# Kernel optimization log

Hardware: AMD Instinct MI355X
Metric: run time of the kernel (lower is better)

The kernel has to match this reference:

```python
import jax, jax.numpy as jnp
import numpy as np

# Qwen3.5 GatedDeltaNet dims
B, T, HID = 2, 2048, 2048
HK, HV, DK, DV, KW = 16, 32, 128, 128, 4   # k-heads, v-heads, head dims, conv kernel
R = HV // HK                                # GQA repeat factor = 2
KEY_DIM = HK * DK                           # 2048
VAL_DIM = HV * DV                           # 4096
CONV_DIM = 2 * KEY_DIM + VAL_DIM            # 8192
EPS = 1e-6


def setup_inputs() -> dict:
    key = jax.random.key(0)
    ks = jax.random.split(key, 10)
    w = lambda k, shape, s=0.02: (jax.random.normal(k, shape) * s).astype(jnp.float32)
    A = jax.random.uniform(ks[8], (HV,), minval=1e-3, maxval=16.0)
    return {
        "hidden_states": jax.random.normal(ks[0], (B, T, HID), jnp.float32),
        "W_qkv": w(ks[1], (HID, CONV_DIM)),
        "W_z": w(ks[2], (HID, VAL_DIM)),
        "W_b": w(ks[3], (HID, HV)),
        "W_a": w(ks[4], (HID, HV)),
        "conv_w": w(ks[5], (CONV_DIM, KW), 0.5),   # depthwise causal conv taps
        "dt_bias": jnp.ones((HV,), jnp.float32),
        "A_log": jnp.log(A).astype(jnp.float32),
        "norm_weight": jnp.ones((DV,), jnp.float32),
        "W_out": w(ks[9], (VAL_DIM, HID)),
    }


def _forward(hidden_states, W_qkv, W_z, W_b, W_a, conv_w, dt_bias, A_log, norm_weight, W_out):
    x = hidden_states
    # --- projections ---
    qkv = x @ W_qkv                                    # [B,T,CONV_DIM]
    z = x @ W_z                                        # [B,T,VAL_DIM]
    beta = jax.nn.sigmoid(x @ W_b)                     # [B,T,HV]
    alpha = x @ W_a                                    # [B,T,HV]
    g = -jnp.exp(A_log) * jax.nn.softplus(alpha + dt_bias)  # [B,T,HV] (log-decay <= 0)

    # --- fix_query_key_value_ordering: per-k-head interleaved layout ---
    qkv = qkv.reshape(B, T, HK, 2 * DK + R * DV)
    q, k, v = jnp.split(qkv, [DK, 2 * DK], axis=3)
    mixed = jnp.concatenate([q.reshape(B, T, -1), k.reshape(B, T, -1), v.reshape(B, T, -1)], axis=-1)

    # --- causal depthwise short conv (kernel 4) + SiLU ---
    xp = jnp.pad(mixed, ((0, 0), (KW - 1, 0), (0, 0)))
    conv = sum(conv_w[:, i] * xp[:, i:i + T, :] for i in range(KW))
    conv = jax.nn.silu(conv)

    q, k, v = jnp.split(conv, [KEY_DIM, 2 * KEY_DIM], axis=-1)
    q = q.reshape(B, T, HK, DK)
    k = k.reshape(B, T, HK, DK)
    v = v.reshape(B, T, HV, DV)
    gate = z.reshape(B, T, HV, DV)

    # GQA: repeat q,k heads to match v heads
    q = jnp.repeat(q, R, axis=2)                       # [B,T,HV,DK]
    k = jnp.repeat(k, R, axis=2)

    # l2-norm q,k (use_qk_l2norm_in_kernel=True) and default scale 1/sqrt(DK)
    q = q / jnp.sqrt(jnp.sum(q * q, axis=-1, keepdims=True) + 1e-6)
    k = k / jnp.sqrt(jnp.sum(k * k, axis=-1, keepdims=True) + 1e-6)
    q = q * (DK ** -0.5)

    # --- gated delta rule recurrence (scan over time) ---
    # state S: [B,HV,DK,DV];  S_t = a_t*S_{t-1} + k_t (beta_t*(v_t - (a_t*S_{t-1})^T k_t))^T
    def step(S, inp):
        qt, kt, vt, gt, bt = inp                       # [B,HV,DK],[B,HV,DK],[B,HV,DV],[B,HV],[B,HV]
        S = S * jnp.exp(gt)[:, :, None, None]
        kv = jnp.einsum('bhk,bhkv->bhv', kt, S)
        delta = bt[..., None] * (vt - kv)              # [B,HV,DV]
        S = S + kt[..., None] * delta[:, :, None, :]
        o = jnp.einsum('bhk,bhkv->bhv', qt, S)
        return S, o

    tfirst = lambda a: jnp.moveaxis(a, 1, 0)           # [T,B,...]
    S0 = jnp.zeros((B, HV, DK, DV), q.dtype)
    _, o = jax.lax.scan(step, S0, (tfirst(q), tfirst(k), tfirst(v), tfirst(g), tfirst(beta)))
    o = jnp.moveaxis(o, 0, 1)                          # [B,T,HV,DV]

    # --- gated RMSNorm: rmsnorm(o) * silu(gate) * weight ---
    var = jnp.mean(o * o, axis=-1, keepdims=True)
    o = o * jax.lax.rsqrt(var + EPS)
    o = o * jax.nn.silu(gate)
    o = o * norm_weight

    return o.reshape(B, T, VAL_DIM) @ W_out            # [B,T,HID]


def reference(hidden_states, W_qkv, W_z, W_b, W_a, conv_w, dt_bias, A_log, norm_weight, W_out):
    return _forward(hidden_states, W_qkv, W_z, W_b, W_a, conv_w, dt_bias, A_log, norm_weight, W_out)
```

## Files before the change

### kernel.cpp

```cpp
#include <hip/hip_runtime.h>


#define T_LEN 2048
#define MROWS 4096
#define CPAD 65

typedef __bf16 bf16x8 __attribute__((ext_vector_type(8)));
typedef float f32x4 __attribute__((ext_vector_type(4)));

#define MFMA(a, b, c) __builtin_amdgcn_mfma_f32_16x16x32_bf16((a), (b), (c), 0, 0, 0)

__device__ __forceinline__ unsigned short f2bf(float f) {
  unsigned int u = __float_as_uint(f);
  unsigned int r = (u + 0x7fffu + ((u >> 16) & 1u)) >> 16;
  return (unsigned short)r;
}
__device__ __forceinline__ float bf2f(unsigned short u) {
  return __uint_as_float(((unsigned int)u) << 16);
}
__device__ __forceinline__ void gload_lds16(const void* g, void* l) {
  __builtin_amdgcn_global_load_lds(
      (const __attribute__((address_space(1))) unsigned int*)g,
      (__attribute__((address_space(3))) unsigned int*)l, 16, 0, 0);
}

__global__ __launch_bounds__(256) void f32_to_bf16_vec(const float* __restrict__ src,
                                                       unsigned short* __restrict__ dst,
                                                       int n4) {
  int i = blockIdx.x * 256 + threadIdx.x;
  if (i >= n4) return;
  float4 v = ((const float4*)src)[i];
  ushort4 o;
  o.x = f2bf(v.x); o.y = f2bf(v.y); o.z = f2bf(v.z); o.w = f2bf(v.w);
  ((ushort4*)dst)[i] = o;
}

__global__ __launch_bounds__(256) void transpose_f2b(const float* __restrict__ src,
                                                     unsigned short* __restrict__ dst,
                                                     int R, int C) {
  __shared__ float tile[32][33];
  int tx = threadIdx.x & 31, ty = threadIdx.x >> 5;
  int c0 = blockIdx.x * 32, r0 = blockIdx.y * 32;
  #pragma unroll
  for (int i = ty; i < 32; i += 8)
    tile[i][tx] = src[(size_t)(r0 + i) * C + c0 + tx];
  __syncthreads();
  #pragma unroll
  for (int i = ty; i < 32; i += 8)
    dst[(size_t)(c0 + i) * R + r0 + tx] = f2bf(tile[tx][i]);
}

template <int OUTBF, int BN>
__global__ __launch_bounds__(512, 2) void gemm256(const unsigned short* __restrict__ A, int lda,
                                                  const unsigned short* __restrict__ Bt, int ldb,
                                                  void* __restrict__ Cv, int ldc,
                                                  int M, int N, int K) {
  constexpr int BUFSZ = 16384 + BN * 64;
  constexpr int BISS = BN / 64;
  constexpr int IS = 4 + BISS;
  constexpr int WMv = (BN == 256) ? 2 : 4;
  constexpr int MSUB = 256 / (WMv * 16);
  constexpr int MSPAN = 256 / WMv;

  __shared__ unsigned short lds[2 * BUFSZ];

  const int mtiles = M >> 8;
  const int nwg = gridDim.x;
  const int orig = blockIdx.x;
  const int q = nwg >> 3, r = nwg & 7;
  const int xcd = orig & 7, idx = orig >> 3;
  const int swz = (xcd < r ? xcd * (q + 1) : r * (q + 1) + (xcd - r) * q) + idx;
  const int m0 = (swz % mtiles) * 256;
  const int n0 = (swz / mtiles) * BN;

  const int tid = threadIdx.x, lane = tid & 63, wv = tid >> 6;
  const int wm = (BN == 256) ? (wv >> 2) : (wv >> 1);
  const int wn = (BN == 256) ? (wv & 3) : (wv & 1);
  const int l15 = lane & 15, l4 = lane >> 4;

  f32x4 acc[MSUB][4];
  #pragma unroll
  for (int i = 0; i < MSUB; i++)
    #pragma unroll
    for (int j = 0; j < 4; j++) acc[i][j] = f32x4{0.f, 0.f, 0.f, 0.f};

  const int NT = K >> 6;

  auto STAGE = [&](int kt) {
    unsigned short* base = lds + (kt & 1) * BUFSZ;
    const int k0 = kt << 6;
    #pragma unroll
    for (int is = 0; is < 4; is++) {
      int ow = is * 8192 + wv * 1024;
      int o = ow + lane * 16;
      int row = o >> 7, colB = o & 127;
      int scol = colB ^ ((row & 7) << 4);
      gload_lds16(A + (size_t)(m0 + row) * lda + k0 + (scol >> 1), base + (ow >> 1));
    }
    #pragma unroll
    for (int is = 0; is < BISS; is++) {
      int ow = is * 8192 + wv * 1024;
      int o = ow + lane * 16;
      int row = o >> 7, colB = o & 127;
      int scol = colB ^ ((row & 7) << 4);
      gload_lds16(Bt + (size_t)(n0 + row) * ldb + k0 + (scol >> 1), base + 16384 + (ow >> 1));
    }
  };

  STAGE(0);
  if (NT > 1) STAGE(1);
  if constexpr (IS == 8) asm volatile("s_waitcnt vmcnt(8)" ::: "memory");
  else                   asm volatile("s_waitcnt vmcnt(6)" ::: "memory");
  __builtin_amdgcn_sched_barrier(0);
  __builtin_amdgcn_s_barrier();
  __builtin_amdgcn_sched_barrier(0);

  for (int t = 0; t < NT; t++) {
    const unsigned short* Abuf = lds + (t & 1) * BUFSZ;
    const unsigned short* Bbuf = Abuf + 16384;
    bf16x8 bF[4][2];
    #pragma unroll
    for (int n = 0; n < 4; n++) {
      int rb = wn * 64 + n * 16 + l15;
      int sw = (rb & 7) << 4;
      #pragma unroll
      for (int ks = 0; ks < 2; ks++) {
        int colB = (ks * 32 + l4 * 8) * 2;
        bF[n][ks] = *(const bf16x8*)(Bbuf + rb * 64 + ((colB ^ sw) >> 1));
      }
    }
    __builtin_amdgcn_s_setprio(1);
    #pragma unroll
    for (int m = 0; m < MSUB; m++) {
      int ra = wm * MSPAN + m * 16 + l15;
      int sw = (ra & 7) << 4;
      int c0b = l4 * 16;
      bf16x8 a0 = *(const bf16x8*)(Abuf + ra * 64 + ((c0b ^ sw) >> 1));
      bf16x8 a1 = *(const bf16x8*)(Abuf + ra * 64 + (((64 + c0b) ^ sw) >> 1));
      #pragma unroll
      for (int n = 0; n < 4; n++) {
        acc[m][n] = MFMA(a0, bF[n][0], acc[m][n]);
        acc[m][n] = MFMA(a1, bF[n][1], acc[m][n]);
      }
    }
    __builtin_amdgcn_s_setprio(0);
    __builtin_amdgcn_sched_barrier(0);
    __builtin_amdgcn_s_barrier();
    __builtin_amdgcn_sched_barrier(0);
    if (t + 2 < NT) STAGE(t + 2);
    if (t + 1 < NT) {
      if (t + 2 < NT) {
        if constexpr (IS == 8) asm volatile("s_waitcnt vmcnt(8)" ::: "memory");
        else                   asm volatile("s_waitcnt vmcnt(6)" ::: "memory");
      } else {
        asm volatile("s_waitcnt vmcnt(0)" ::: "memory");
      }
      __builtin_amdgcn_sched_barrier(0);
      __builtin_amdgcn_s_barrier();
      __builtin_amdgcn_sched_barrier(0);
    }
  }

  #pragma unroll
  for (int m = 0; m < MSUB; m++) {
    int grow = m0 + wm * MSPAN + m * 16 + l4 * 4;
    #pragma unroll
    for (int n = 0; n < 4; n++) {
      int gcol = n0 + wn * 64 + n * 16 + l15;
      if (OUTBF) {
        unsigned short* cp = (unsigned short*)Cv + (size_t)grow * ldc + gcol;
        #pragma unroll
        for (int rr = 0; rr < 4; rr++) cp[(size_t)rr * ldc] = f2bf(acc[m][n][rr]);
      } else {
        float* cp = (float*)Cv + (size_t)grow * ldc + gcol;
        #pragma unroll
        for (int rr = 0; rr < 4; rr++) cp[(size_t)rr * ldc] = acc[m][n][rr];
      }
    }
  }
}

template <int OUTBF>
__global__ __launch_bounds__(256) void gemm_bf16(const unsigned short* __restrict__ A, int lda,
                                                 const unsigned short* __restrict__ Bt, int ldb,
                                                 void* __restrict__ Cv, int ldc,
                                                 int M, int N, int K) {
  __shared__ unsigned short As[128 * 64];
  __shared__ unsigned short Bs[128 * 64];
  const int tid = threadIdx.x, lane = tid & 63, wv = tid >> 6;
  const int wr = wv >> 1, wc = wv & 1;
  const int m0 = blockIdx.y * 128, n0 = blockIdx.x * 128;
  const int lrow8 = lane >> 3;
  const int lk8 = (lane & 7) * 8;

  f32x4 acc[4][4];
  #pragma unroll
  for (int i = 0; i < 4; i++)
    #pragma unroll
    for (int j = 0; j < 4; j++) acc[i][j] = f32x4{0.f, 0.f, 0.f, 0.f};

  for (int k0 = 0; k0 < K; k0 += 64) {
    #pragma unroll
    for (int j = 0; j < 4; ++j) {
      int chunk = j * 4 + wv;
      int r = chunk * 8 + lrow8;
      gload_lds16(A + (size_t)(m0 + r) * lda + k0 + lk8, (void*)(As + chunk * 512));
      gload_lds16(Bt + (size_t)(n0 + r) * ldb + k0 + lk8, (void*)(Bs + chunk * 512));
    }
    __syncthreads();
    #pragma unroll
    for (int half = 0; half < 2; ++half) {
      int ko = half * 32 + (lane >> 4) * 8;
      bf16x8 af[4], bfr[4];
      #pragma unroll
      for (int i = 0; i < 4; i++) {
        int ra = wr * 64 + i * 16 + (lane & 15);
        af[i] = *(const bf16x8*)(As + ra * 64 + ko);
        int rb = wc * 64 + i * 16 + (lane & 15);
        bfr[i] = *(const bf16x8*)(Bs + rb * 64 + ko);
      }
      #pragma unroll
      for (int i = 0; i < 4; i++)
        #pragma unroll
        for (int j = 0; j < 4; j++)
          acc[i][j] = MFMA(af[i], bfr[j], acc[i][j]);
    }
    __syncthreads();
  }
  int cr4 = (lane >> 4) * 4;
  int cc = lane & 15;
  #pragma unroll
  for (int i = 0; i < 4; i++) {
    int row = m0 + wr * 64 + i * 16 + cr4;
    #pragma unroll
    for (int j = 0; j < 4; j++) {
      int col = n0 + wc * 64 + j * 16 + cc;
      if (OUTBF) {
        unsigned short* cp = (unsigned short*)Cv + (size_t)row * ldc + col;
        #pragma unroll
        for (int r = 0; r < 4; r++) cp[(size_t)r * ldc] = f2bf(acc[i][j][r]);
      } else {
        float* cp = (float*)Cv + (size_t)row * ldc + col;
        #pragma unroll
        for (int r = 0; r < 4; r++) cp[(size_t)r * ldc] = acc[i][j][r];
      }
    }
  }
}

__global__ __launch_bounds__(256) void beta_g_kernel(const unsigned short* __restrict__ ba,
                                                     const float* __restrict__ A_log,
                                                     const float* __restrict__ dt_bias,
                                                     unsigned short* __restrict__ betab,
                                                     float* __restrict__ g) {
  int i = blockIdx.x * 256 + threadIdx.x;
  int row = i >> 5, hv = i & 31;
  float rb = bf2f(ba[(size_t)row * 128 + hv]);
  float ra = bf2f(ba[(size_t)row * 128 + 32 + hv]);
  betab[i] = f2bf(1.f / (1.f + expf(-rb)));
  float xg = ra + dt_bias[hv];
  float sp = (xg > 20.f) ? xg : log1pf(expf(xg));
  g[i] = -expf(A_log[hv]) * sp;
}

__global__ __launch_bounds__(256) void conv_kernel(const unsigned short* __restrict__ qkv,
                                                   const float* __restrict__ conv_w,
                                                   unsigned short* __restrict__ out) {
  const int seg = blockIdx.x, tt = blockIdx.y, b = blockIdx.z;
  const int tid = threadIdx.x;
  const int c0 = seg * 128;
  const bool isq = seg < 16;
  int scb;
  if (isq) scb = seg * 512;
  else if (seg < 32) scb = (seg - 16) * 512 + 128;
  else scb = ((seg - 32) >> 1) * 512 + 256 + ((seg - 32) & 1) * 128;

  __shared__ unsigned short raw[35][136];
  __shared__ float cw[4][132];

  for (int i = tid; i < 512; i += 256) {
    int cl = i >> 2, tap = i & 3;
    cw[tap][cl] = conv_w[(size_t)(c0 + cl) * 4 + tap];
  }
  const int t0 = tt * 32;
  for (int i = tid; i < 560; i += 256) {
    int row = i >> 4, col = (i & 15) * 8;
    int gt = t0 - 3 + row;
    uint4 v = make_uint4(0u, 0u, 0u, 0u);
    if (gt >= 0) v = *(const uint4*)(qkv + (size_t)(b * T_LEN + gt) * 8192 + scb + col);
    *(uint4*)(&raw[row][col]) = v;
  }
  __syncthreads();
  const int s = tid >> 3, dg = tid & 7;
  union RawU { uint4 v[2]; unsigned short h[16]; };
  RawU u[4];
  #pragma unroll
  for (int i = 0; i < 4; i++) {
    const uint4* p = (const uint4*)&raw[s + i][dg * 16];
    u[i].v[0] = p[0]; u[i].v[1] = p[1];
  }
  float vals[16]; float ss = 0.f;
  #pragma unroll
  for (int j = 0; j < 16; j++) {
    float a = 0.f;
    #pragma unroll
    for (int i = 0; i < 4; i++) a = fmaf(cw[i][dg * 16 + j], bf2f(u[i].h[j]), a);
    a = a / (1.f + expf(-a));
    vals[j] = a; ss += a * a;
  }
  if (seg < 32) {
    ss += __shfl_xor(ss, 1); ss += __shfl_xor(ss, 2); ss += __shfl_xor(ss, 4);
    float sc = rsqrtf(ss + 1e-6f);
    if (isq) sc *= 0.08838834764831845f;
    #pragma unroll
    for (int j = 0; j < 16; j++) vals[j] *= sc;
  }
  union { uint4 v[2]; unsigned short h[16]; } ov;
  #pragma unroll
  for (int j = 0; j < 16; j++) ov.h[j] = f2bf(vals[j]);
  unsigned short* op = out + (size_t)(b * T_LEN + t0 + s) * 8192 + c0 + dg * 16;
  *(uint4*)(op) = ov.v[0];
  *(uint4*)(op + 8) = ov.v[1];
}

__global__ __launch_bounds__(256) void prep_kernel(const unsigned short* __restrict__ conv,
                                                   const float* __restrict__ g,
                                                   const unsigned short* __restrict__ betab,
                                                   unsigned short* __restrict__ M1g,
                                                   unsigned short* __restrict__ M2g,
                                                   unsigned char* __restrict__ vecs) {
  const int c = blockIdx.x, bh = blockIdx.y;
  const int b = bh >> 5, hv = bh & 31, hk = hv >> 1;
  const int bhc = bh * 32 + c;
  const int tid = threadIdx.x, lane = tid & 63, wv = tid >> 6;
  const int r0 = b * T_LEN + c * 64;

  __shared__ unsigned short Kb[128 * 72];
  __shared__ unsigned short Qb[64 * 136];
  __shared__ float Ab[64 * CPAD];
  __shared__ unsigned short Pb[64 * 72];
  __shared__ float Gs[64], Ls[64], SCs[64], BLs[64];

  if (wv == 0) {
    float gt = g[(size_t)(r0 + lane) * 32 + hv];
    #pragma unroll
    for (int d = 1; d < 64; d <<= 1) {
      float o = __shfl_up(gt, (unsigned)d, 64);
      if (lane >= d) gt += o;
    }
    float GC = __shfl(gt, 63, 64);
    float lam = expf(gt);
    float beta = bf2f(betab[(size_t)(r0 + lane) * 32 + hv]);
    Gs[lane] = gt; Ls[lane] = lam;
    SCs[lane] = expf(GC - gt);
    BLs[lane] = beta;
    unsigned short* vb16 = (unsigned short*)(vecs + (size_t)bhc * 272);
    vb16[lane] = f2bf(beta * lam);
    vb16[64 + lane] = f2bf(lam);
    if (lane == 0) *(float*)(vecs + (size_t)bhc * 272 + 256) = expf(GC);
  }
  const unsigned short* Kg = conv + (size_t)r0 * 8192 + 2048 + hk * 128;
  const unsigned short* Qg = conv + (size_t)r0 * 8192 + hk * 128;
  for (int u = tid; u < 1024; u += 256) {
    int row = u >> 4, col = (u & 15) * 8;
    *(uint4*)(&Kb[row * 136 + col]) = *(const uint4*)(Kg + (size_t)row * 8192 + col);
    *(uint4*)(&Qb[row * 136 + col]) = *(const uint4*)(Qg + (size_t)row * 8192 + col);
  }
  __syncthreads();

  {
    f32x4 akk[4], aqk[4];
    #pragma unroll
    for (int st = 0; st < 4; st++) { akk[st] = f32x4{0,0,0,0}; aqk[st] = f32x4{0,0,0,0}; }
    int trow = wv * 16 + (lane & 15);
    int klo = (lane >> 4) * 8;
    #pragma unroll
    for (int ks = 0; ks < 4; ks++) {
      int ko = ks * 32 + klo;
      bf16x8 ak = *(const bf16x8*)(&Kb[trow * 136 + ko]);
      bf16x8 aq = *(const bf16x8*)(&Qb[trow * 136 + ko]);
      #pragma unroll
      for (int st = 0; st < 4; st++) {
        bf16x8 bk = *(const bf16x8*)(&Kb[(st * 16 + (lane & 15)) * 136 + ko]);
        akk[st] = MFMA(ak, bk, akk[st]);
        aqk[st] = MFMA(aq, bk, aqk[st]);
      }
    }
    int orow = wv * 16 + (lane >> 4) * 4;
    int oc = lane & 15;
    #pragma unroll
    for (int st = 0; st < 4; st++)
      #pragma unroll
      for (int r = 0; r < 4; r++) {
        int t = orow + r, ssv = st * 16 + oc;
        float e = expf(fminf(Gs[t] - Gs[ssv], 0.f));
        Ab[t * CPAD + ssv] = (ssv < t) ? BLs[t] * e * akk[st][r] : (ssv == t ? 1.f : 0.f);
        Pb[t * 72 + ssv] = f2bf((ssv <= t) ? e * aqk[st][r] : 0.f);
      }
  }
  __syncthreads();

  {
    unsigned short ktv[32];
    int dk = tid >> 1, tb = (tid & 1) * 32;
    #pragma unroll
    for (int i = 0; i < 32; i++)
      ktv[i] = f2bf(bf2f(Kb[(tb + i) * 136 + dk]) * SCs[tb + i]);
    __syncthreads();
    #pragma unroll
    for (int i = 0; i < 32; i++) Kb[dk * 72 + tb + i] = ktv[i];
  }
  __syncthreads();

  float* XT = (float*)Qb;
  if (wv == 0) {
    XT[lane * CPAD + 0] = (lane == 0) ? 1.f : 0.f;
    for (int t = 1; t < 64; t++) {
      float a0 = 0.f, a1 = 0.f, a2 = 0.f, a3 = 0.f;
      int sI = 0;
      for (; sI + 4 <= t; sI += 4) {
        a0 = fmaf(Ab[t * CPAD + sI],     XT[lane * CPAD + sI],     a0);
        a1 = fmaf(Ab[t * CPAD + sI + 1], XT[lane * CPAD + sI + 1], a1);
        a2 = fmaf(Ab[t * CPAD + sI + 2], XT[lane * CPAD + sI + 2], a2);
        a3 = fmaf(Ab[t * CPAD + sI + 3], XT[lane * CPAD + sI + 3], a3);
      }
      for (; sI < t; sI++) a0 = fmaf(Ab[t * CPAD + sI], XT[lane * CPAD + sI], a0);
      XT[lane * CPAD + t] = ((lane == t) ? 1.f : 0.f) - (a0 + a1 + (a2 + a3));
    }
  }
  __syncthreads();

  unsigned short* XTb = (unsigned short*)Ab;
  for (int e = tid; e < 4096; e += 256) {
    int j = e >> 6, sI = e & 63;
    XTb[j * 72 + sI] = f2bf(XT[j * CPAD + sI]);
  }
  __syncthreads();

  for (int tt = wv * 12; tt < wv * 12 + 12; tt++) {
    f32x4 acc = f32x4{0, 0, 0, 0};
    const unsigned short* Abase;
    int mrow, jc;
    if (tt < 16) { mrow = (tt >> 2) * 16; jc = (tt & 3) * 16; Abase = Pb + mrow * 72; }
    else { int i2 = tt - 16; mrow = (i2 >> 2) * 16; jc = (i2 & 3) * 16; Abase = Kb + mrow * 72; }
    #pragma unroll
    for (int ks = 0; ks < 2; ks++) {
      int so = ks * 32 + (lane >> 4) * 8;
      bf16x8 af = *(const bf16x8*)(Abase + (lane & 15) * 72 + so);
      bf16x8 bfv = *(const bf16x8*)(XTb + (jc + (lane & 15)) * 72 + so);
      acc = MFMA(af, bfv, acc);
    }
    int ro = mrow + (lane >> 4) * 4, co = jc + (lane & 15);
    if (tt < 16) {
      #pragma unroll
      for (int r = 0; r < 4; r++)
        M1g[(size_t)bhc * 4096 + (ro + r) * 64 + co] = f2bf(acc[r]);
    } else {
      #pragma unroll
      for (int r = 0; r < 4; r++)
        M2g[(size_t)bhc * 8192 + (ro + r) * 64 + co] = f2bf(acc[r]);
    }
  }
}

__global__ __launch_bounds__(512) void seq_kernel(unsigned short* __restrict__ conv,
                                                  const unsigned short* __restrict__ M1g,
                                                  const unsigned short* __restrict__ M2g,
                                                  const unsigned char* __restrict__ vecs,
                                                  const unsigned short* __restrict__ betab) {
  const int dvs = blockIdx.x, bh = blockIdx.y;
  const int b = bh >> 5, hv = bh & 31, hk = hv >> 1;
  const int dv0 = dvs * 32;
  const int tid = threadIdx.x, lane = tid & 63, wv = tid >> 6;

  __shared__ unsigned short Kb[64 * 136], Qb[64 * 136];
  __shared__ float Sf[128 * 36];
  __shared__ unsigned short S0T[32 * 136];
  __shared__ unsigned short rhsT[32 * 72];

  for (int i = tid; i < 128 * 36; i += 512) Sf[i] = 0.f;
  for (int i = tid; i < 32 * 136; i += 512) S0T[i] = 0;
  __syncthreads();

  const int l15 = lane & 15, l4 = lane >> 4;
  const int trt = (wv >> 1) * 16;
  const int tct = (wv & 1) * 16;

  for (int c = 0; c < 32; c++) {
    const int r0 = b * T_LEN + c * 64;
    const int bhc = bh * 32 + c;
    const unsigned char* vb = vecs + (size_t)bhc * 272;
    const unsigned short* vb16 = (const unsigned short*)vb;
    #pragma unroll
    for (int j = 0; j < 2; j++) {
      int u = tid * 2 + j;
      int row = u >> 4, col = (u & 15) * 8;
      uint4 kv = *(const uint4*)(conv + (size_t)(r0 + row) * 8192 + 2048 + hk * 128 + col);
      uint4 qv = *(const uint4*)(conv + (size_t)(r0 + row) * 8192 + hk * 128 + col);
      *(uint4*)(&Kb[row * 136 + col]) = kv;
      float lam = bf2f(vb16[64 + row]);
      union { uint4 u4; unsigned short h[8]; } qq; qq.u4 = qv;
      #pragma unroll
      for (int e = 0; e < 8; e++) qq.h[e] = f2bf(bf2f(qq.h[e]) * lam);
      *(uint4*)(&Qb[row * 136 + col]) = qq.u4;
    }
    __syncthreads();
    {
      f32x4 acc = f32x4{0, 0, 0, 0};
      #pragma unroll
      for (int ks = 0; ks < 4; ks++) {
        int ko = ks * 32 + l4 * 8;
        bf16x8 af = *(const bf16x8*)(&Kb[(trt + l15) * 136 + ko]);
        bf16x8 bfv = *(const bf16x8*)(&S0T[(tct + l15) * 136 + ko]);
        acc = MFMA(af, bfv, acc);
      }
      #pragma unroll
      for (int r = 0; r < 4; r++) {
        int tl = trt + l4 * 4 + r;
        int t = r0 + tl;
        float beta = bf2f(betab[(size_t)t * 32 + hv]);
        float bl = bf2f(vb16[tl]);
        float vv = bf2f(conv[(size_t)t * 8192 + 4096 + hv * 128 + dv0 + tct + l15]);
        rhsT[(tct + l15) * 72 + tl] = f2bf(beta * vv - bl * acc[r]);
      }
    }
    __syncthreads();
    {
      f32x4 acc = f32x4{0, 0, 0, 0};
      const unsigned short* m1b = M1g + (size_t)bhc * 4096;
      #pragma unroll
      for (int ks = 0; ks < 2; ks++) {
        int so = ks * 32 + l4 * 8;
        union { uint4 u4; bf16x8 h; } af;
        af.u4 = *(const uint4*)(m1b + (trt + l15) * 64 + so);
        bf16x8 bfv = *(const bf16x8*)(&rhsT[(tct + l15) * 72 + so]);
        acc = MFMA(af.h, bfv, acc);
      }
      #pragma unroll
      for (int ks = 0; ks < 4; ks++) {
        int ko = ks * 32 + l4 * 8;
        bf16x8 af = *(const bf16x8*)(&Qb[(trt + l15) * 136 + ko]);
        bf16x8 bfv = *(const bf16x8*)(&S0T[(tct + l15) * 136 + ko]);
        acc = MFMA(af, bfv, acc);
      }
      #pragma unroll
      for (int r = 0; r < 4; r++) {
        int t = r0 + trt + l4 * 4 + r;
        conv[(size_t)t * 8192 + 4096 + hv * 128 + dv0 + tct + l15] = f2bf(acc[r]);
      }
    }
    {
      float lamC = *(const float*)(vb + 256);
      f32x4 sacc[2];
      const unsigned short* m2b = M2g + (size_t)bhc * 8192;
      const int dkb = wv * 16;
      #pragma unroll
      for (int dt = 0; dt < 2; dt++) {
        int dvb = dt * 16;
        f32x4 a;
        #pragma unroll
        for (int r = 0; r < 4; r++) a[r] = lamC * Sf[(dkb + l4 * 4 + r) * 36 + dvb + l15];
        #pragma unroll
        for (int ks = 0; ks < 2; ks++) {
          int so = ks * 32 + l4 * 8;
          union { uint4 u4; bf16x8 h; } af;
          af.u4 = *(const uint4*)(m2b + (dkb + l15) * 64 + so);
          bf16x8 bfv = *(const bf16x8*)(&rhsT[(dvb + l15) * 72 + so]);
          a = MFMA(af.h, bfv, a);
        }
        sacc[dt] = a;
      }
      __syncthreads();
      #pragma unroll
      for (int dt = 0; dt < 2; dt++) {
        int dvb = dt * 16;
        #pragma unroll
        for (int r = 0; r < 4; r++) {
          int dk = dkb + l4 * 4 + r, dvl = dvb + l15;
          Sf[dk * 36 + dvl] = sacc[dt][r];
          S0T[dvl * 136 + dk] = f2bf(sacc[dt][r]);
        }
      }
    }
    __syncthreads();
  }
}

__global__ __launch_bounds__(256) void rmsgate_kernel(unsigned short* __restrict__ conv,
                                                      const unsigned short* __restrict__ zg,
                                                      const float* __restrict__ nw) {
  int wid = blockIdx.x * 4 + (threadIdx.x >> 6);
  int lane = threadIdx.x & 63;
  int row = wid >> 5, hv = wid & 31;
  unsigned short* op = conv + (size_t)row * 8192 + 4096 + hv * 128;
  float o0 = bf2f(op[lane]), o1 = bf2f(op[64 + lane]);
  float ss = o0 * o0 + o1 * o1;
  #pragma unroll
  for (int m = 1; m < 64; m <<= 1) ss += __shfl_xor(ss, m);
  float r = rsqrtf(ss * (1.f / 128.f) + 1e-6f);
  const unsigned short* zp = zg + (size_t)row * 4096 + hv * 128;
  float g0 = bf2f(zp[lane]), g1 = bf2f(zp[64 + lane]);
  g0 = g0 / (1.f + expf(-g0));
  g1 = g1 / (1.f + expf(-g1));
  op[lane] = f2bf(o0 * r * g0 * nw[lane]);
  op[64 + lane] = f2bf(o1 * r * g1 * nw[64 + lane]);
}

extern "C" void kernel_launch(void* const* d_in, const int* in_sizes, int n_in,
                              void* d_out, int out_size, void* d_ws, size_t ws_size,
                              hipStream_t stream) {
  (void)in_sizes; (void)n_in; (void)out_size;
  const float* x       = (const float*)d_in[0];
  const float* W_qkv   = (const float*)d_in[1];
  const float* W_z     = (const float*)d_in[2];
  const float* W_b     = (const float*)d_in[3];
  const float* W_a     = (const float*)d_in[4];
  const float* conv_w  = (const float*)d_in[5];
  const float* dt_bias = (const float*)d_in[6];
  const float* A_log   = (const float*)d_in[7];
  const float* nw      = (const float*)d_in[8];
  const float* W_out   = (const float*)d_in[9];
  float* out = (float*)d_out;

  const size_t NEED = 169115648ULL;
  if (ws_size < NEED) return;

  char* ws = (char*)d_ws;
  unsigned short* qkv_bf = (unsigned short*)(ws + 0);
  unsigned short* M1g    = (unsigned short*)(ws + 0);
  unsigned short* M2g    = (unsigned short*)(ws + 16777216);
  unsigned short* WoutT  = (unsigned short*)(ws + 0);
  unsigned short* zg     = (unsigned short*)(ws + 67108864);
  unsigned short* WzT    = (unsigned short*)(ws + 100663296);
  unsigned short* x_bf   = (unsigned short*)(ws + 100663296 + 16777216);
  unsigned short* WqkvT  = (unsigned short*)(ws + 100663296 + 33554432);
  unsigned short* WbaT   = (unsigned short*)(ws + 100663296 + 33554432);
  unsigned short* ba     = (unsigned short*)(ws + 100663296 + 34078720);
  unsigned short* convb  = (unsigned short*)(ws + 100663296);
  unsigned short* betab  = (unsigned short*)(ws + 167772160);
  float* gbuf            = (float*)(ws + 168034304);
  unsigned char* vecs    = (unsigned char*)(ws + 168558592);

  const int M = MROWS;

  f32_to_bf16_vec<<<(M * 2048 / 4) / 256, 256, 0, stream>>>(x, x_bf, M * 2048 / 4);
  transpose_f2b<<<dim3(8192 / 32, 2048 / 32), 256, 0, stream>>>(W_qkv, WqkvT, 2048, 8192);
  transpose_f2b<<<dim3(4096 / 32, 2048 / 32), 256, 0, stream>>>(W_z, WzT, 2048, 4096);

  gemm256<1, 256><<<512, 512, 0, stream>>>(x_bf, 2048, WqkvT, 2048, qkv_bf, 8192, M, 8192, 2048);

  transpose_f2b<<<dim3(1, 64), 256, 0, stream>>>(W_b, WbaT, 2048, 32);
  transpose_f2b<<<dim3(1, 64), 256, 0, stream>>>(W_a, WbaT + (size_t)32 * 2048, 2048, 32);

  gemm256<1, 256><<<256, 512, 0, stream>>>(x_bf, 2048, WzT, 2048, zg, 4096, M, 4096, 2048);
  gemm_bf16<1><<<dim3(1, M / 128), 256, 0, stream>>>(x_bf, 2048, WbaT, 2048, ba, 128, M, 128, 2048);

  beta_g_kernel<<<(M * 32) / 256, 256, 0, stream>>>(ba, A_log, dt_bias, betab, gbuf);

  conv_kernel<<<dim3(64, 64, 2), 256, 0, stream>>>(qkv_bf, conv_w, convb);

  prep_kernel<<<dim3(32, 64), 256, 0, stream>>>(convb, gbuf, betab, M1g, M2g, vecs);

  seq_kernel<<<dim3(4, 64), 512, 0, stream>>>(convb, M1g, M2g, vecs, betab);

  rmsgate_kernel<<<32768, 256, 0, stream>>>(convb, zg, nw);

  transpose_f2b<<<dim3(2048 / 32, 4096 / 32), 256, 0, stream>>>(W_out, WoutT, 4096, 2048);
  gemm256<0, 128><<<256, 512, 0, stream>>>(convb + 4096, 8192, WoutT, 4096, out, 2048, M, 2048, 4096);
}
```

Baseline: 718.8 us.

## Replace serial triangular inverse in prep kernel with blocked MFMA inversion

```diff
diff --git a/kernel.cpp b/kernel.cpp
--- a/kernel.cpp
+++ b/kernel.cpp
@@ -3,7 +3,6 @@
 
 #define T_LEN 2048
 #define MROWS 4096
-#define CPAD 65
 
 typedef __bf16 bf16x8 __attribute__((ext_vector_type(8)));
 typedef float f32x4 __attribute__((ext_vector_type(4)));
@@ -334,12 +333,18 @@
   const int bhc = bh * 32 + c;
   const int tid = threadIdx.x, lane = tid & 63, wv = tid >> 6;
   const int r0 = b * T_LEN + c * 64;
+  const int l15 = lane & 15, l4 = lane >> 4;
 
   __shared__ unsigned short Kb[128 * 72];
-  __shared__ unsigned short Qb[64 * 136];
-  __shared__ float Ab[64 * CPAD];
+  __shared__ unsigned short QbX[64 * 136];
+  __shared__ unsigned short Lbf[64 * 72];
   __shared__ unsigned short Pb[64 * 72];
-  __shared__ float Gs[64], Ls[64], SCs[64], BLs[64];
+  __shared__ unsigned short WT[3 * 16 * 40];
+  __shared__ float Gs[64], SCs[64], BLs[64];
+
+  unsigned short* Qb = QbX;
+  unsigned short* XTb = QbX;
+  unsigned short* Xdrow = QbX + 4608;
 
   if (wv == 0) {
     float gt = g[(size_t)(r0 + lane) * 32 + hv];
@@ -351,7 +356,7 @@
     float GC = __shfl(gt, 63, 64);
     float lam = expf(gt);
     float beta = bf2f(betab[(size_t)(r0 + lane) * 32 + hv]);
-    Gs[lane] = gt; Ls[lane] = lam;
+    Gs[lane] = gt;
     SCs[lane] = expf(GC - gt);
     BLs[lane] = beta;
     unsigned short* vb16 = (unsigned short*)(vecs + (size_t)bhc * 272);
@@ -372,8 +377,8 @@
     f32x4 akk[4], aqk[4];
     #pragma unroll
     for (int st = 0; st < 4; st++) { akk[st] = f32x4{0,0,0,0}; aqk[st] = f32x4{0,0,0,0}; }
-    int trow = wv * 16 + (lane & 15);
-    int klo = (lane >> 4) * 8;
+    int trow = wv * 16 + l15;
+    int klo = l4 * 8;
     #pragma unroll
     for (int ks = 0; ks < 4; ks++) {
       int ko = ks * 32 + klo;
@@ -381,59 +386,96 @@
       bf16x8 aq = *(const bf16x8*)(&Qb[trow * 136 + ko]);
       #pragma unroll
       for (int st = 0; st < 4; st++) {
-        bf16x8 bk = *(const bf16x8*)(&Kb[(st * 16 + (lane & 15)) * 136 + ko]);
+        bf16x8 bk = *(const bf16x8*)(&Kb[(st * 16 + l15) * 136 + ko]);
         akk[st] = MFMA(ak, bk, akk[st]);
         aqk[st] = MFMA(aq, bk, aqk[st]);
       }
     }
-    int orow = wv * 16 + (lane >> 4) * 4;
-    int oc = lane & 15;
+    int orow = wv * 16 + l4 * 4;
+    int oc = l15;
     #pragma unroll
     for (int st = 0; st < 4; st++)
       #pragma unroll
       for (int r = 0; r < 4; r++) {
         int t = orow + r, ssv = st * 16 + oc;
         float e = expf(fminf(Gs[t] - Gs[ssv], 0.f));
-        Ab[t * CPAD + ssv] = (ssv < t) ? BLs[t] * e * akk[st][r] : (ssv == t ? 1.f : 0.f);
+        Lbf[t * 72 + ssv] = f2bf((ssv < t) ? BLs[t] * e * akk[st][r] : 0.f);
         Pb[t * 72 + ssv] = f2bf((ssv <= t) ? e * aqk[st][r] : 0.f);
       }
   }
   __syncthreads();
 
+  unsigned short ktv[32];
   {
-    unsigned short ktv[32];
     int dk = tid >> 1, tb = (tid & 1) * 32;
     #pragma unroll
     for (int i = 0; i < 32; i++)
       ktv[i] = f2bf(bf2f(Kb[(tb + i) * 136 + dk]) * SCs[tb + i]);
-    __syncthreads();
+    for (int u = tid; u < 896; u += 256) {
+      *(uint4*)(&QbX[u * 8]) = make_uint4(0u, 0u, 0u, 0u);
+    }
+    for (int u = tid; u < 240; u += 256) {
+      *(uint4*)(&WT[u * 8]) = make_uint4(0u, 0u, 0u, 0u);
+    }
+  }
+  __syncthreads();
+
+  {
+    int dk = tid >> 1, tb = (tid & 1) * 32;
     #pragma unroll
     for (int i = 0; i < 32; i++) Kb[dk * 72 + tb + i] = ktv[i];
   }
+  {
+    const int w16 = wv * 16;
+    const int cc = l15;
+    float xr[16];
+    #pragma unroll
+    for (int t = 0; t < 16; t++) {
+      float acc = (cc == t) ? 1.f : 0.f;
+      union { uint4 v[2]; unsigned short h[16]; } rw;
+      const uint4* p = (const uint4*)(&Lbf[(w16 + t) * 72 + w16]);
+      rw.v[0] = p[0]; rw.v[1] = p[1];
+      #pragma unroll
+      for (int s = 0; s < 16; s++) {
+        if (s < t) acc = fmaf(-bf2f(rw.h[s]), xr[s], acc);
+      }
+      xr[t] = acc;
+    }
+    if (lane < 16) {
+      #pragma unroll
+      for (int t = 0; t < 16; t++) {
+        unsigned short v = f2bf(xr[t]);
+        XTb[(w16 + cc) * 72 + w16 + t] = v;
+        Xdrow[wv * 640 + t * 40 + cc] = v;
+      }
+    }
+  }
   __syncthreads();
 
-  float* XT = (float*)Qb;
-  if (wv == 0) {
-    XT[lane * CPAD + 0] = (lane == 0) ? 1.f : 0.f;
-    for (int t = 1; t < 64; t++) {
-      float a0 = 0.f, a1 = 0.f, a2 = 0.f, a3 = 0.f;
-      int sI = 0;
-      for (; sI + 4 <= t; sI += 4) {
-        a0 = fmaf(Ab[t * CPAD + sI],     XT[lane * CPAD + sI],     a0);
-        a1 = fmaf(Ab[t * CPAD + sI + 1], XT[lane * CPAD + sI + 1], a1);
-        a2 = fmaf(Ab[t * CPAD + sI + 2], XT[lane * CPAD + sI + 2], a2);
-        a3 = fmaf(Ab[t * CPAD + sI + 3], XT[lane * CPAD + sI + 3], a3);
-      }
-      for (; sI < t; sI++) a0 = fmaf(Ab[t * CPAD + sI], XT[lane * CPAD + sI], a0);
-      XT[lane * CPAD + t] = ((lane == t) ? 1.f : 0.f) - (a0 + a1 + (a2 + a3));
-    }
-  }
-  __syncthreads();
-
-  unsigned short* XTb = (unsigned short*)Ab;
-  for (int e = tid; e < 4096; e += 256) {
-    int j = e >> 6, sI = e & 63;
-    XTb[j * 72 + sI] = f2bf(XT[j * CPAD + sI]);
+  if (wv < 3) {
+    const int j = wv;
+    for (int i = j + 1; i < 4; i++) {
+      f32x4 w_ = f32x4{0.f, 0.f, 0.f, 0.f};
+      #pragma unroll
+      for (int ks = 0; ks < 2; ks++) {
+        int so = ks * 32 + l4 * 8;
+        bf16x8 af = *(const bf16x8*)(&Lbf[(i * 16 + l15) * 72 + so]);
+        bf16x8 bfv = *(const bf16x8*)(&XTb[(j * 16 + l15) * 72 + so]);
+        w_ = MFMA(af, bfv, w_);
+      }
+      #pragma unroll
+      for (int r = 0; r < 4; r++)
+        WT[j * 640 + l15 * 40 + l4 * 4 + r] = f2bf(-w_[r]);
+      f32x4 xij = f32x4{0.f, 0.f, 0.f, 0.f};
+      {
+        bf16x8 af = *(const bf16x8*)(&Xdrow[i * 640 + l15 * 40 + l4 * 8]);
+        bf16x8 bfv = *(const bf16x8*)(&WT[j * 640 + l15 * 40 + l4 * 8]);
+        xij = MFMA(af, bfv, xij);
+      }
+      #pragma unroll
+      for (int r = 0; r < 4; r++)
+        XTb[(j * 16 + l15) * 72 + i * 16 + l4 * 4 + r] = f2bf(xij[r]);
+    }
   }
   __syncthreads();
 
@@ -445,12 +487,12 @@
     else { int i2 = tt - 16; mrow = (i2 >> 2) * 16; jc = (i2 & 3) * 16; Abase = Kb + mrow * 72; }
     #pragma unroll
     for (int ks = 0; ks < 2; ks++) {
-      int so = ks * 32 + (lane >> 4) * 8;
-      bf16x8 af = *(const bf16x8*)(Abase + (lane & 15) * 72 + so);
-      bf16x8 bfv = *(const bf16x8*)(XTb + (jc + (lane & 15)) * 72 + so);
+      int so = ks * 32 + l4 * 8;
+      bf16x8 af = *(const bf16x8*)(Abase + l15 * 72 + so);
+      bf16x8 bfv = *(const bf16x8*)(&XTb[(jc + l15) * 72 + so]);
       acc = MFMA(af, bfv, acc);
     }
-    int ro = mrow + (lane >> 4) * 4, co = jc + (lane & 15);
+    int ro = mrow + l4 * 4, co = jc + l15;
     if (tt < 16) {
       #pragma unroll
       for (int r = 0; r < 4; r++)
```

Measured after the change: 621.7 us. 13.5% less time.
